# Performance work log

Hardware: AMD Instinct MI355X
Metric: run time of the kernel (lower is better)

Reference implementation:

```python
import jax, jax.numpy as jnp
import numpy as np

D_MODEL = 1024
HEADS = 16
HEAD_DIM = D_MODEL // HEADS


def setup_inputs() -> dict:
    key = jax.random.key(0)
    ks = jax.random.split(key, 6)
    B, S, D = 2, 2048, D_MODEL
    scale = 1.0 / np.sqrt(D)
    x = jax.random.normal(ks[0], (B, S, D), dtype=jnp.float32)
    mask = jax.random.randint(ks[1], (B, S), 0, 2, dtype=jnp.int32)
    Wq = jax.random.normal(ks[2], (D, D), dtype=jnp.float32) * scale
    Wk = jax.random.normal(ks[3], (D, D), dtype=jnp.float32) * scale
    Wv = jax.random.normal(ks[4], (D, D), dtype=jnp.float32) * scale
    Wp = jax.random.normal(ks[5], (D, D), dtype=jnp.float32) * scale
    zb = jnp.zeros((D,), dtype=jnp.float32)
    return {"x": x, "mask": mask, "Wq": Wq, "bq": zb, "Wk": Wk, "bk": zb,
            "Wv": Wv, "bv": zb, "Wp": Wp, "bp": zb}


def reference(x, mask, Wq, bq, Wk, bk, Wv, bv, Wp, bp):
    B, S, D = x.shape
    H, Dh = HEADS, HEAD_DIM

    def split_heads(t):  # [B,S,D] -> [B,H,S,Dh]
        return t.reshape(B, S, H, Dh).transpose(0, 2, 1, 3)

    q = split_heads(x @ Wq + bq)
    k = split_heads(x @ Wk + bk)
    v = split_heads(x @ Wv + bv)

    att = jnp.einsum('bhqd,bhkd->bhqk', q, k) / jnp.sqrt(jnp.float32(Dh))
    # key-padding mask: [B,S] -> [B,1,1,S]; masked positions -> -inf
    m = (mask[:, None, None, :] != 0)
    att = jnp.where(m, att, -jnp.inf)
    att = jax.nn.softmax(att, axis=-1)
    # rows that were fully masked produce NaN -> zero them (masked_fill(isnan, 0))
    att = jnp.where(jnp.isnan(att), 0.0, att)

    y = jnp.einsum('bhqk,bhkd->bhqd', att, v)  # [B,H,S,Dh]
    y = y.transpose(0, 2, 1, 3).reshape(B, S, D)
    return y @ Wp + bp
```

## Files before the change

kernel.cpp:

```cpp
#include <hip/hip_runtime.h>
#include <math.h>

#define D_MODEL 1024
#define HEADS 16
#define HEAD_DIM 64
#define SEQ 2048
#define BATCH 2
#define KVT 64
#define QTILE 128
#define SCALE_Q 0.18033688f

typedef __attribute__((ext_vector_type(8))) short bf16x8;
typedef __attribute__((ext_vector_type(4))) float f32x4;
typedef __attribute__((ext_vector_type(16))) float f32x16;

__device__ __forceinline__ short f2bf(float f) {
    union { float f; unsigned u; } v; v.f = f;
    unsigned r = (v.u + 0x7FFFu + ((v.u >> 16) & 1u)) >> 16;
    return (short)r;
}

__device__ __forceinline__ unsigned cvt_pk_bf16(float lo, float hi) {
    unsigned r;
    asm("v_cvt_pk_bf16_f32 %0, %1, %2" : "=v"(r) : "v"(lo), "v"(hi));
    return r;
}

__device__ __forceinline__ float fexp2(float x) {
    float r;
    asm("v_exp_f32 %0, %1" : "=v"(r) : "v"(x));
    return r;
}

__global__ __launch_bounds__(256) void prep(
    const float* __restrict__ x, const float* __restrict__ Wq,
    const float* __restrict__ Wk, const float* __restrict__ Wv,
    const float* __restrict__ Wp, const int* __restrict__ mask,
    short* __restrict__ xb, short* __restrict__ Wqkvt,
    short* __restrict__ Wpt, float* __restrict__ maskf) {
    __shared__ float t[32][33];
    const int bid = blockIdx.x;
    if (bid < 2048) {
        const int i = bid * 256 + threadIdx.x;
        float4 a = ((const float4*)x)[2 * i];
        float4 b = ((const float4*)x)[2 * i + 1];
        short r[8] = {f2bf(a.x), f2bf(a.y), f2bf(a.z), f2bf(a.w),
                      f2bf(b.x), f2bf(b.y), f2bf(b.z), f2bf(b.w)};
        *(uint4*)(xb + 8 * i) = *(uint4*)r;
    } else if (bid < 6144) {
        const int tt = bid - 2048;
        const int z = tt >> 10;
        const int rem = tt & 1023;
        const float* W = z == 0 ? Wq : z == 1 ? Wk : z == 2 ? Wv : Wp;
        short* dst = (z < 3) ? Wqkvt + (size_t)z * 1024 * 1024 : Wpt;
        const int n0 = (rem & 31) * 32, k0 = (rem >> 5) * 32;
        const int tx = threadIdx.x & 31, ty = threadIdx.x >> 5;
#pragma unroll
        for (int j = 0; j < 4; ++j)
            t[ty + j * 8][tx] = W[(size_t)(k0 + ty + j * 8) * 1024 + n0 + tx];
        __syncthreads();
#pragma unroll
        for (int j = 0; j < 4; ++j) {
            const int n = ty + j * 8;
            dst[(size_t)(n0 + n) * 1024 + k0 + tx] = f2bf(t[tx][n]);
        }
    } else {
        const int i = (bid - 6144) * 256 + threadIdx.x;
        maskf[i] = mask[i] ? 0.f : -INFINITY;
    }
}

template <int MODE>
__global__ __launch_bounds__(256) void mfma_gemm(
    const short* __restrict__ A, const short* __restrict__ Bt,
    const float* __restrict__ b0, const float* __restrict__ b1,
    const float* __restrict__ b2, float* __restrict__ outf,
    short* __restrict__ o0, short* __restrict__ o1, short* __restrict__ o2,
    int M, int N, int K) {
    __shared__ short As[2 * 128 * 32];
    __shared__ short Bs[2 * 128 * 32];

    const int tid = threadIdx.x;
    const int wave = tid >> 6, lane = tid & 63;
    const int l15 = lane & 15, lhi = lane >> 4;
    const int wm = wave >> 1, wn = wave & 1;
    const int bm0 = blockIdx.y * 128, bn0 = blockIdx.x * 128;

    f32x4 acc[4][4];
#pragma unroll
    for (int m = 0; m < 4; ++m)
#pragma unroll
        for (int n = 0; n < 4; ++n) acc[m][n] = (f32x4){0.f, 0.f, 0.f, 0.f};

#define STAGE_G(buf, kt_)                                                         \
    {                                                                             \
        const int k0 = (kt_) * 32;                                                \
        _Pragma("unroll") for (int p = 0; p < 2; ++p) {                           \
            const int o = (wave * 2 + p) * 64 + lane;                             \
            const int r = o >> 2;                                                 \
            const int gs = (o & 3) ^ ((r >> 1) & 3);                              \
            __builtin_amdgcn_global_load_lds(                                     \
                (const __attribute__((address_space(1))) void*)(                  \
                    A + (size_t)(bm0 + r) * K + k0 + gs * 8),                     \
                (__attribute__((address_space(3))) void*)(                        \
                    As + (size_t)(buf) * 4096 + (wave * 2 + p) * 512),            \
                16, 0, 0);                                                        \
            __builtin_amdgcn_global_load_lds(                                     \
                (const __attribute__((address_space(1))) void*)(                  \
                    Bt + (size_t)(bn0 + r) * K + k0 + gs * 8),                    \
                (__attribute__((address_space(3))) void*)(                        \
                    Bs + (size_t)(buf) * 4096 + (wave * 2 + p) * 512),            \
                16, 0, 0);                                                        \
        }                                                                         \
    }

    const int NT = K / 32;
    STAGE_G(0, 0);
    __syncthreads();
    for (int kt = 0; kt < NT; ++kt) {
        const int cur = kt & 1;
        if (kt + 1 < NT) STAGE_G((kt + 1) & 1, kt + 1);
        bf16x8 af[4], bf[4];
        const int sg = (lhi ^ ((l15 >> 1) & 3)) * 16;
#pragma unroll
        for (int m = 0; m < 4; ++m)
            af[m] = *(const bf16x8*)((char*)As + cur * 8192 +
                                     (wm * 64 + m * 16 + l15) * 64 + sg);
#pragma unroll
        for (int n = 0; n < 4; ++n)
            bf[n] = *(const bf16x8*)((char*)Bs + cur * 8192 +
                                     (wn * 64 + n * 16 + l15) * 64 + sg);
        __builtin_amdgcn_s_setprio(1);
#pragma unroll
        for (int m = 0; m < 4; ++m)
#pragma unroll
            for (int n = 0; n < 4; ++n)
                acc[m][n] = __builtin_amdgcn_mfma_f32_16x16x32_bf16(af[m], bf[n], acc[m][n], 0, 0, 0);
        __builtin_amdgcn_s_setprio(0);
        __syncthreads();
    }
#undef STAGE_G

    const int which = (MODE == 1) ? (bn0 >> 10) : 0;
#pragma unroll
    for (int m = 0; m < 4; ++m) {
#pragma unroll
        for (int n = 0; n < 4; ++n) {
            const int col = bn0 + wn * 64 + n * 16 + l15;
            if (MODE == 0) {
#pragma unroll
                for (int rr = 0; rr < 4; ++rr) {
                    const int row = bm0 + wm * 64 + m * 16 + lhi * 4 + rr;
                    outf[(size_t)row * N + col] = acc[m][n][rr] + b0[col];
                }
            } else {
                const int cc = col & 1023;
                const int h = cc >> 6, dh = cc & 63;
                const int row0 = bm0 + wm * 64 + m * 16 + lhi * 4;
                const int b = row0 >> 11, s0 = row0 & (SEQ - 1);
                if (which == 2) {
                    const float bias = b2[cc];
                    uint2 w;
                    w.x = cvt_pk_bf16(acc[m][n][0] + bias, acc[m][n][1] + bias);
                    w.y = cvt_pk_bf16(acc[m][n][2] + bias, acc[m][n][3] + bias);
                    *(uint2*)(o2 + ((size_t)(b * HEADS + h) * HEAD_DIM + dh) * SEQ + s0) = w;
                } else {
                    const float bias = (which == 0 ? b0 : b1)[cc];
                    short* dst = which == 0 ? o0 : o1;
#pragma unroll
                    for (int rr = 0; rr < 4; ++rr) {
                        float v = acc[m][n][rr] + bias;
                        if (which == 0) v *= SCALE_Q;
                        dst[(((size_t)(b * HEADS + h)) * SEQ + s0 + rr) * HEAD_DIM + dh] = f2bf(v);
                    }
                }
            }
        }
    }
}

__global__ __launch_bounds__(256, 2) void flash_attn(
    const short* __restrict__ Q, const short* __restrict__ K,
    const short* __restrict__ Vt, const float* __restrict__ maskf,
    short* __restrict__ Y) {
    __shared__ unsigned char kt[2][KVT * 128];
    __shared__ unsigned char vt[2][HEAD_DIM * 128];
    __shared__ unsigned char pb[4][32 * 128];

    const int tid = threadIdx.x;
    const int wave = tid >> 6;
    const int lane = tid & 63;
    const int l31 = lane & 31;
    const int lh = lane >> 5;
    const int psw = (l31 & 7) << 4;

    const int nwg = gridDim.x;
    const int wg = blockIdx.x;
    const int swz = (wg & 7) * (nwg >> 3) + (wg >> 3);
    const int qt = swz & 15;
    const int bh = swz >> 4;
    const int b = bh >> 4;

    const int q0 = qt * QTILE + wave * 32;

    const short* Qp = Q + ((size_t)bh * SEQ + q0 + l31) * HEAD_DIM;
    bf16x8 qf[4];
#pragma unroll
    for (int s = 0; s < 4; ++s)
        qf[s] = *(const bf16x8*)(Qp + 16 * s + 8 * lh);

    const unsigned char* Kb8 = (const unsigned char*)(K + (size_t)bh * SEQ * HEAD_DIM);
    const unsigned char* Vb8 = (const unsigned char*)(Vt + (size_t)bh * HEAD_DIM * SEQ);
    const float* mb = maskf + b * SEQ;

#define STAGE(buf, kvi)                                                            \
    {                                                                              \
        const unsigned char* kbase = Kb8 + (size_t)(kvi) * KVT * 128;              \
        const unsigned char* vbase = Vb8 + (size_t)(kvi) * 128;                    \
        _Pragma("unroll") for (int p = 0; p < 2; ++p) {                            \
            const int o = (wave * 2 + p) * 64 + lane;                              \
            const int row = o >> 3;                                                \
            const int inner = (o & 7) * 16;                                        \
            const int src = inner ^ ((row & 7) << 4);                              \
            __builtin_amdgcn_global_load_lds(                                      \
                (const __attribute__((address_space(1))) void*)(                   \
                    kbase + row * 128 + src),                                      \
                (__attribute__((address_space(3))) void*)(                         \
                    &kt[buf][(wave * 2 + p) * 1024]),                              \
                16, 0, 0);                                                         \
            __builtin_amdgcn_global_load_lds(                                      \
                (const __attribute__((address_space(1))) void*)(                   \
                    vbase + (size_t)row * (SEQ * 2) + src),                        \
                (__attribute__((address_space(3))) void*)(                         \
                    &vt[buf][(wave * 2 + p) * 1024]),                              \
                16, 0, 0);                                                         \
        }                                                                          \
    }

    f32x16 accO[2];
    float mrow = -30000.f, lrow = 0.f;
#pragma unroll
    for (int d = 0; d < 2; ++d)
#pragma unroll
        for (int r = 0; r < 16; ++r) accO[d][r] = 0.f;

    STAGE(0, 0);
    __syncthreads();

    for (int kv = 0; kv < SEQ / KVT; ++kv) {
        const int cur = kv & 1;
        if (kv + 1 < SEQ / KVT) STAGE((kv + 1) & 1, kv + 1);

        const int k0 = kv * KVT;

        f32x16 accS[2];
#pragma unroll
        for (int kb = 0; kb < 2; ++kb)
#pragma unroll
            for (int r = 0; r < 16; ++r) accS[kb][r] = 0.f;
#pragma unroll
        for (int s = 0; s < 4; ++s) {
            bf16x8 kf[2];
#pragma unroll
            for (int kb = 0; kb < 2; ++kb) {
                const int row = 32 * kb + l31;
                kf[kb] = *(const bf16x8*)(kt[cur] + row * 128 +
                                          ((32 * s + 16 * lh) ^ ((row & 7) << 4)));
            }
            __builtin_amdgcn_s_setprio(1);
#pragma unroll
            for (int kb = 0; kb < 2; ++kb)
                accS[kb] = __builtin_amdgcn_mfma_f32_32x32x16_bf16(kf[kb], qf[s], accS[kb], 0, 0, 0);
            __builtin_amdgcn_s_setprio(0);
        }

#pragma unroll
        for (int kb = 0; kb < 2; ++kb)
#pragma unroll
            for (int g = 0; g < 4; ++g) {
                const f32x4 ma = *(const f32x4*)(mb + k0 + 32 * kb + 8 * g + 4 * lh);
#pragma unroll
                for (int j = 0; j < 4; ++j) accS[kb][4 * g + j] += ma[j];
            }

        float mx[2];
#pragma unroll
        for (int kb = 0; kb < 2; ++kb) {
            float a0 = fmaxf(fmaxf(accS[kb][0], accS[kb][1]), fmaxf(accS[kb][2], accS[kb][3]));
            float a1 = fmaxf(fmaxf(accS[kb][4], accS[kb][5]), fmaxf(accS[kb][6], accS[kb][7]));
            float a2 = fmaxf(fmaxf(accS[kb][8], accS[kb][9]), fmaxf(accS[kb][10], accS[kb][11]));
            float a3 = fmaxf(fmaxf(accS[kb][12], accS[kb][13]), fmaxf(accS[kb][14], accS[kb][15]));
            mx[kb] = fmaxf(fmaxf(a0, a1), fmaxf(a2, a3));
        }
        float smax = fmaxf(mx[0], mx[1]);
        smax = fmaxf(smax, __shfl_xor(smax, 32));

        if (!__all(smax <= mrow + 11.5f)) {
            const float mn = fmaxf(mrow, smax);
            const float alpha = fexp2(mrow - mn);
            lrow *= alpha;
#pragma unroll
            for (int d = 0; d < 2; ++d)
#pragma unroll
                for (int r = 0; r < 16; ++r) accO[d][r] *= alpha;
            mrow = mn;
        }

        float rs = 0.f;
#pragma unroll
        for (int kb = 0; kb < 2; ++kb)
#pragma unroll
            for (int r = 0; r < 16; ++r) {
                const float pv = fexp2(accS[kb][r] - mrow);
                accS[kb][r] = pv;
                rs += pv;
            }
        rs += __shfl_xor(rs, 32);
        lrow += rs;

#pragma unroll
        for (int kb = 0; kb < 2; ++kb)
#pragma unroll
            for (int g = 0; g < 4; ++g) {
                uint2 w;
                w.x = cvt_pk_bf16(accS[kb][4 * g], accS[kb][4 * g + 1]);
                w.y = cvt_pk_bf16(accS[kb][4 * g + 2], accS[kb][4 * g + 3]);
                *(uint2*)(pb[wave] + l31 * 128 +
                          ((64 * kb + 16 * g + 8 * lh) ^ psw)) = w;
            }

#pragma unroll
        for (int t = 0; t < 4; ++t) {
            const bf16x8 pf = *(const bf16x8*)(pb[wave] + l31 * 128 +
                                               ((32 * t + 16 * lh) ^ psw));
            bf16x8 vf[2];
#pragma unroll
            for (int db = 0; db < 2; ++db) {
                const int row = 32 * db + l31;
                vf[db] = *(const bf16x8*)(vt[cur] + row * 128 +
                                          ((32 * t + 16 * lh) ^ ((row & 7) << 4)));
            }
            __builtin_amdgcn_s_setprio(1);
#pragma unroll
            for (int db = 0; db < 2; ++db)
                accO[db] = __builtin_amdgcn_mfma_f32_32x32x16_bf16(vf[db], pf, accO[db], 0, 0, 0);
            __builtin_amdgcn_s_setprio(0);
        }
        __syncthreads();
    }
#undef STAGE

    const float inv = (lrow > 0.f) ? 1.f / lrow : 0.f;
    const int qg = q0 + l31;
    short* Yp = Y + ((size_t)b * SEQ + qg) * D_MODEL + (bh & 15) * HEAD_DIM;
#pragma unroll
    for (int db = 0; db < 2; ++db)
#pragma unroll
        for (int g = 0; g < 4; ++g) {
            uint2 w;
            w.x = cvt_pk_bf16(accO[db][4 * g] * inv, accO[db][4 * g + 1] * inv);
            w.y = cvt_pk_bf16(accO[db][4 * g + 2] * inv, accO[db][4 * g + 3] * inv);
            *(uint2*)(Yp + 32 * db + 8 * g + 4 * lh) = w;
        }
}

extern "C" void kernel_launch(void* const* d_in, const int* in_sizes, int n_in,
                              void* d_out, int out_size, void* d_ws, size_t ws_size,
                              hipStream_t stream) {
    const float* x    = (const float*)d_in[0];
    const int*   mask = (const int*)  d_in[1];
    const float* Wq   = (const float*)d_in[2];
    const float* bq   = (const float*)d_in[3];
    const float* Wk   = (const float*)d_in[4];
    const float* bk   = (const float*)d_in[5];
    const float* Wv   = (const float*)d_in[6];
    const float* bv   = (const float*)d_in[7];
    const float* Wp   = (const float*)d_in[8];
    const float* bp   = (const float*)d_in[9];
    float* out = (float*)d_out;

    short* ws    = (short*)d_ws;
    short* xb    = ws;
    short* Wqkvt = xb + ((size_t)4 << 20);
    short* Wpt   = Wqkvt + ((size_t)3 << 20);
    short* Qb    = Wpt + ((size_t)1 << 20);
    short* Kb    = Qb + ((size_t)4 << 20);
    short* Vtb   = Kb + ((size_t)4 << 20);
    short* Yb    = Vtb + ((size_t)4 << 20);
    float* maskf = (float*)(Yb + ((size_t)4 << 20));

    const int M = BATCH * SEQ;

    prep<<<dim3(6160), 256, 0, stream>>>(x, Wq, Wk, Wv, Wp, mask,
                                         xb, Wqkvt, Wpt, maskf);

    mfma_gemm<1><<<dim3(3 * D_MODEL / 128, M / 128), 256, 0, stream>>>(
        xb, Wqkvt, bq, bk, bv, nullptr, Qb, Kb, Vtb, M, 3 * D_MODEL, D_MODEL);

    flash_attn<<<dim3(BATCH * HEADS * (SEQ / QTILE)), 256, 0, stream>>>(Qb, Kb, Vtb, maskf, Yb);

    mfma_gemm<0><<<dim3(D_MODEL / 128, M / 128), 256, 0, stream>>>(
        Yb, Wpt, bp, bp, bp, out, nullptr, nullptr, nullptr, M, D_MODEL, D_MODEL);
}
```

Measured before the change: 135.4 us.

## Use column-chunk LDS layout for K/V/P tiles and raise flash_attn occupancy

Replaces the XOR-swizzled row-major LDS layout for K, V and the P scratch tile with a chunk-major layout. Each 16-byte column chunk of all rows is stored contiguously, so MFMA operand reads become linear per-lane accesses and need no swizzle arithmetic. The global loads now gather one 16-byte chunk per row, which is less coalesced per instruction. Launch bounds also request 3 workgroups per CU, which caps registers per thread and may cause spills.

After: 143.8 us. 6.2% more time.

```diff
diff --git a/kernel.cpp b/kernel.cpp
--- a/kernel.cpp
+++ b/kernel.cpp
@@ -179,7 +179,7 @@
     }
 }
 
-__global__ __launch_bounds__(256, 2) void flash_attn(
+__global__ __launch_bounds__(256, 3) void flash_attn(
     const short* __restrict__ Q, const short* __restrict__ K,
     const short* __restrict__ Vt, const float* __restrict__ maskf,
     short* __restrict__ Y) {
@@ -192,7 +192,6 @@
     const int lane = tid & 63;
     const int l31 = lane & 31;
     const int lh = lane >> 5;
-    const int psw = (l31 & 7) << 4;
 
     const int nwg = gridDim.x;
     const int wg = blockIdx.x;
@@ -218,21 +217,16 @@
         const unsigned char* kbase = Kb8 + (size_t)(kvi) * KVT * 128;              \
         const unsigned char* vbase = Vb8 + (size_t)(kvi) * 128;                    \
         _Pragma("unroll") for (int p = 0; p < 2; ++p) {                            \
-            const int o = (wave * 2 + p) * 64 + lane;                              \
-            const int row = o >> 3;                                                \
-            const int inner = (o & 7) * 16;                                        \
-            const int src = inner ^ ((row & 7) << 4);                              \
+            const int g = wave * 2 + p;                                            \
             __builtin_amdgcn_global_load_lds(                                      \
                 (const __attribute__((address_space(1))) void*)(                   \
-                    kbase + row * 128 + src),                                      \
-                (__attribute__((address_space(3))) void*)(                         \
-                    &kt[buf][(wave * 2 + p) * 1024]),                              \
+                    kbase + lane * 128 + g * 16),                                  \
+                (__attribute__((address_space(3))) void*)(&kt[buf][g * 1024]),     \
                 16, 0, 0);                                                         \
             __builtin_amdgcn_global_load_lds(                                      \
                 (const __attribute__((address_space(1))) void*)(                   \
-                    vbase + (size_t)row * (SEQ * 2) + src),                        \
-                (__attribute__((address_space(3))) void*)(                         \
-                    &vt[buf][(wave * 2 + p) * 1024]),                              \
+                    vbase + (size_t)lane * (SEQ * 2) + g * 16),                    \
+                (__attribute__((address_space(3))) void*)(&vt[buf][g * 1024]),     \
                 16, 0, 0);                                                         \
         }                                                                          \
     }
@@ -262,11 +256,9 @@
         for (int s = 0; s < 4; ++s) {
             bf16x8 kf[2];
 #pragma unroll
-            for (int kb = 0; kb < 2; ++kb) {
-                const int row = 32 * kb + l31;
-                kf[kb] = *(const bf16x8*)(kt[cur] + row * 128 +
-                                          ((32 * s + 16 * lh) ^ ((row & 7) << 4)));
-            }
+            for (int kb = 0; kb < 2; ++kb)
+                kf[kb] = *(const bf16x8*)(kt[cur] + (2 * s + lh) * 1024 +
+                                          (32 * kb + l31) * 16);
             __builtin_amdgcn_s_setprio(1);
 #pragma unroll
             for (int kb = 0; kb < 2; ++kb)
@@ -325,21 +317,17 @@
                 uint2 w;
                 w.x = cvt_pk_bf16(accS[kb][4 * g], accS[kb][4 * g + 1]);
                 w.y = cvt_pk_bf16(accS[kb][4 * g + 2], accS[kb][4 * g + 3]);
-                *(uint2*)(pb[wave] + l31 * 128 +
-                          ((64 * kb + 16 * g + 8 * lh) ^ psw)) = w;
+                *(uint2*)(pb[wave] + (4 * kb + g) * 512 + l31 * 16 + lh * 8) = w;
             }
 
 #pragma unroll
         for (int t = 0; t < 4; ++t) {
-            const bf16x8 pf = *(const bf16x8*)(pb[wave] + l31 * 128 +
-                                               ((32 * t + 16 * lh) ^ psw));
+            const bf16x8 pf = *(const bf16x8*)(pb[wave] + (2 * t + lh) * 512 + l31 * 16);
             bf16x8 vf[2];
 #pragma unroll
-            for (int db = 0; db < 2; ++db) {
-                const int row = 32 * db + l31;
-                vf[db] = *(const bf16x8*)(vt[cur] + row * 128 +
-                                          ((32 * t + 16 * lh) ^ ((row & 7) << 4)));
-            }
+            for (int db = 0; db < 2; ++db)
+                vf[db] = *(const bf16x8*)(vt[cur] + (2 * t + lh) * 1024 +
+                                          (32 * db + l31) * 16);
             __builtin_amdgcn_s_setprio(1);
 #pragma unroll
             for (int db = 0; db < 2; ++db)
```
